# Kernel tuning notes

Hardware: AMD Instinct MI355X
Metric: run time of the kernel (lower is better)

## Reference

```python
import jax, jax.numpy as jnp
import numpy as np

C_SKIP = 64       # channels of a and of b (concat -> 128)
C_OUT = 64
N = 131072        # coarse nodes
E = 1048576       # directed edges (avg degree 8)
N_FINE = 4 * N    # fine mesh nodes after unpool
K = 3 * N_FINE    # unpool scatter assignments


def setup_inputs() -> dict:
    key = jax.random.key(0)
    ks = jax.random.split(key, 9)
    return {
        "a": jax.random.normal(ks[0], (C_SKIP, N), dtype=jnp.float32),
        "b": jax.random.normal(ks[1], (C_SKIP, N), dtype=jnp.float32),
        "W_self": jax.random.normal(ks[2], (C_OUT, 2 * C_SKIP), dtype=jnp.float32) * 0.05,
        "W_neigh": jax.random.normal(ks[3], (C_OUT, 2 * C_SKIP), dtype=jnp.float32) * 0.05,
        "bias": jax.random.normal(ks[4], (C_OUT,), dtype=jnp.float32) * 0.05,
        "gather_index": jax.random.randint(ks[5], (E,), 0, N),
        "reduce_index": jax.random.randint(ks[6], (E,), 0, N),
        "unpool_src": jax.random.randint(ks[7], (K,), 0, N),
        "unpool_dst": jax.random.randint(ks[8], (K,), 0, N_FINE),
    }


def reference(a, b, W_self, W_neigh, bias, gather_index, reduce_index, unpool_src, unpool_dst):
    # concat skip connection along channel dim (-2)
    x = jnp.concatenate((a, b), axis=-2)                  # [C_in, N]
    n = x.shape[-1]
    # GraphConv: gather source features along edges, segment-sum into targets
    msgs = x[:, gather_index]                              # [C_in, E]
    agg = jax.ops.segment_sum(msgs.T, reduce_index, num_segments=n).T  # [C_in, N]
    h = W_self @ x + W_neigh @ agg + bias[:, None]         # [C_out, N]
    h = jax.nn.relu(h)
    # GraphUnpool with reduce='amax': scatter-max coarse features to fine mesh
    out = jnp.zeros((h.shape[0], 4 * n), dtype=h.dtype)
    out = out.at[:, unpool_dst].max(h[:, unpool_src])      # [C_out, N_fine]
    return out
```

## Files before the change

### kernel.cpp

```cpp
#include <hip/hip_runtime.h>
#include <stdint.h>

constexpr int NN = 131072;
constexpr int EE = 1048576;
constexpr int NF = 4 * NN;
constexpr int KK = 3 * NF;

constexpr int NBLK = 256;
constexpr int SH_E = 6;
constexpr int SH_K = 7;
constexpr int NB_E = NN >> SH_E;
constexpr int NB_K = NF >> SH_K;
constexpr int EPT_E = EE / NBLK / 256;
constexpr int EPT_K = KK / NBLK / 256;
constexpr int CAP_E = 2048;
constexpr int CAP_K = 1024;
constexpr int KOFF = NB_E * NBLK;
constexpr int NH   = NB_E * NBLK + NB_K * NBLK;
constexpr int NSCB = NH / 2048;

typedef __attribute__((ext_vector_type(8))) short bf16x8;
typedef __attribute__((ext_vector_type(4))) float f32x4;

__device__ inline uint32_t bf16rn(float f) {
    uint32_t u = __float_as_uint(f);
    return (u + 0x7FFFu + ((u >> 16) & 1u)) >> 16;
}
__device__ inline uint32_t pack2(float lo, float hi) {
    return bf16rn(lo) | (bf16rn(hi) << 16);
}
__device__ inline float bf_lo(uint32_t v) { return __uint_as_float(v << 16); }
__device__ inline float bf_hi(uint32_t v) { return __uint_as_float(v & 0xFFFF0000u); }

__global__ __launch_bounds__(256) void k_transpose(
    const float* __restrict__ a, const float* __restrict__ b,
    uint32_t* __restrict__ xTb)
{
    __shared__ float tile[128][33];
    int i0 = blockIdx.x * 32;
    for (int f = threadIdx.x; f < 128 * 32; f += 256) {
        int c = f >> 5, j = f & 31;
        const float* src = (c < 64) ? a : b;
        tile[c][j] = src[(size_t)(c & 63) * NN + i0 + j];
    }
    __syncthreads();
    for (int f = threadIdx.x; f < 64 * 32; f += 256) {
        int p = f & 63, j = f >> 6;
        xTb[(size_t)(i0 + j) * 64 + p] = pack2(tile[2 * p][j], tile[2 * p + 1][j]);
    }
}

template<int NB, int EPT>
__device__ void pass1_body(const int* __restrict__ idx, int shift,
                           int* __restrict__ histG, int blk, int* hist)
{
    for (int f = threadIdx.x; f < NB; f += 256) hist[f] = 0;
    __syncthreads();
    int base = blk * (256 * EPT);
#pragma unroll
    for (int u = 0; u < EPT; ++u) {
        int b = idx[base + u * 256 + threadIdx.x] >> shift;
        atomicAdd(&hist[b], 1);
    }
    __syncthreads();
    for (int f = threadIdx.x; f < NB; f += 256)
        histG[f * NBLK + blk] = hist[f];
}

__global__ __launch_bounds__(256) void k_pass1(
    const int* __restrict__ reduce_i, const int* __restrict__ up_dst,
    int* __restrict__ histG)
{
    __shared__ int hist[NB_K];
    if (blockIdx.x < NBLK)
        pass1_body<NB_E, EPT_E>(reduce_i, SH_E, histG, blockIdx.x, hist);
    else
        pass1_body<NB_K, EPT_K>(up_dst, SH_K, histG + KOFF, blockIdx.x - NBLK, hist);
}

__global__ __launch_bounds__(256) void k_bsum(
    const int* __restrict__ cnt, int* __restrict__ bsum)
{
    __shared__ int s[256];
    int base = blockIdx.x * 2048;
    int sum = 0;
    for (int j = threadIdx.x; j < 2048; j += 256) sum += cnt[base + j];
    s[threadIdx.x] = sum;
    __syncthreads();
    for (int o = 128; o > 0; o >>= 1) {
        if (threadIdx.x < o) s[threadIdx.x] += s[threadIdx.x + o];
        __syncthreads();
    }
    if (threadIdx.x == 0) bsum[blockIdx.x] = s[0];
}

__global__ __launch_bounds__(256) void k_final(
    int* __restrict__ offs, const int* __restrict__ bsum)
{
    __shared__ int ts[256];
    int partial = 0;
    for (int i = threadIdx.x; i < blockIdx.x; i += 256) partial += bsum[i];
    ts[threadIdx.x] = partial;
    __syncthreads();
    for (int o = 128; o > 0; o >>= 1) {
        if (threadIdx.x < o) ts[threadIdx.x] += ts[threadIdx.x + o];
        __syncthreads();
    }
    int bb = ts[0];
    __syncthreads();

    int base = blockIdx.x * 2048 + threadIdx.x * 8;
    int loc[8];
    int sum = 0;
#pragma unroll
    for (int u = 0; u < 8; ++u) {
        int v = offs[base + u];
        loc[u] = sum;
        sum += v;
    }
    ts[threadIdx.x] = sum;
    __syncthreads();
    for (int o = 1; o < 256; o <<= 1) {
        int v = (threadIdx.x >= o) ? ts[threadIdx.x - o] : 0;
        __syncthreads();
        ts[threadIdx.x] += v;
        __syncthreads();
    }
    int texc = (threadIdx.x == 0) ? 0 : ts[threadIdx.x - 1];
#pragma unroll
    for (int u = 0; u < 8; ++u) offs[base + u] = bb + texc + loc[u];
    if (blockIdx.x == gridDim.x - 1 && threadIdx.x == 255) offs[NH] = bb + ts[255];
}

template<int NB, int EPT>
__device__ void pass2_body(const int* __restrict__ idx,
                           const int* __restrict__ payload, int shift,
                           const int* __restrict__ offsG, int sub,
                           uint32_t* __restrict__ pairs, int blk, int* curs)
{
    for (int f = threadIdx.x; f < NB; f += 256)
        curs[f] = offsG[f * NBLK + blk] - sub;
    __syncthreads();
    int lmask = (1 << shift) - 1;
    int base = blk * (256 * EPT);
#pragma unroll
    for (int u = 0; u < EPT; ++u) {
        int e = base + u * 256 + threadIdx.x;
        int bk = idx[e];
        int pos = atomicAdd(&curs[bk >> shift], 1);
        pairs[pos] = (uint32_t)payload[e] | ((uint32_t)(bk & lmask) << 17);
    }
}

__global__ __launch_bounds__(256) void k_pass2(
    const int* __restrict__ reduce_i, const int* __restrict__ gather_i,
    const int* __restrict__ up_dst, const int* __restrict__ up_src,
    const int* __restrict__ offs,
    uint32_t* __restrict__ pairsE, uint32_t* __restrict__ pairsK)
{
    __shared__ int curs[NB_K];
    if (blockIdx.x < NBLK)
        pass2_body<NB_E, EPT_E>(reduce_i, gather_i, SH_E, offs, 0,
                                pairsE, blockIdx.x, curs);
    else
        pass2_body<NB_K, EPT_K>(up_dst, up_src, SH_K, offs + KOFF, EE,
                                pairsK, blockIdx.x - NBLK, curs);
}

__global__ __launch_bounds__(256) void k_aggcsr(
    const uint32_t* __restrict__ xTb, const int* __restrict__ offsE,
    const uint32_t* __restrict__ pairsE, uint32_t* __restrict__ aggB)
{
    __shared__ uint32_t list[CAP_E];
    __shared__ int offs[65];
    __shared__ int curs[64];
    __shared__ int cnt_s;
    int bin = blockIdx.x;
    if (threadIdx.x == 0) {
        int beg = offsE[bin * NBLK];
        cnt_s = min(offsE[(bin + 1) * NBLK] - beg, CAP_E);
    }
    if (threadIdx.x < 64) curs[threadIdx.x] = 0;
    __syncthreads();
    int beg = offsE[bin * NBLK];
    int cnt = cnt_s;
    for (int i = threadIdx.x; i < cnt; i += 256)
        atomicAdd(&curs[(pairsE[beg + i] >> 17) & 63], 1);
    __syncthreads();
    if (threadIdx.x == 0) {
        int run = 0;
        for (int j = 0; j < 64; ++j) {
            offs[j] = run;
            run += curs[j];
            curs[j] = offs[j];
        }
        offs[64] = run;
    }
    __syncthreads();
    for (int i = threadIdx.x; i < cnt; i += 256) {
        uint32_t u = pairsE[beg + i];
        int p = atomicAdd(&curs[(u >> 17) & 63], 1);
        list[p] = u;
    }
    __syncthreads();

    int w = threadIdx.x >> 6, lane = threadIdx.x & 63;
    int n0 = w * 16, n1 = n0 + 16;
    int e0 = offs[n0], e1 = offs[n1];
    size_t rowbase = (size_t)(bin * 64) * 64 + lane;
    float sx = 0.f, sy = 0.f;
    int cur = n0;
    for (int e = e0; e < e1; e += 16) {
        int nb = e1 - e;
        uint32_t pr[16], v[16];
#pragma unroll
        for (int j = 0; j < 16; ++j)
            pr[j] = list[e + ((j < nb) ? j : (nb - 1))];
#pragma unroll
        for (int j = 0; j < 16; ++j)
            v[j] = xTb[(size_t)(pr[j] & 0x1FFFF) * 64 + lane];
#pragma unroll
        for (int j = 0; j < 16; ++j) {
            if (j < nb) {
                int d = (pr[j] >> 17) & 63;
                if (d != cur) {
                    aggB[rowbase + (size_t)cur * 64] = pack2(sx, sy);
                    for (int z = cur + 1; z < d; ++z)
                        aggB[rowbase + (size_t)z * 64] = 0u;
                    cur = d;
                    sx = 0.f; sy = 0.f;
                }
                sx += bf_lo(v[j]);
                sy += bf_hi(v[j]);
            }
        }
    }
    aggB[rowbase + (size_t)cur * 64] = pack2(sx, sy);
    for (int z = cur + 1; z < n1; ++z)
        aggB[rowbase + (size_t)z * 64] = 0u;
}

__global__ __launch_bounds__(256) void k_gemm(
    const uint32_t* __restrict__ xTb, const uint32_t* __restrict__ aggB,
    const float* __restrict__ Wself, const float* __restrict__ Wneigh,
    const float* __restrict__ bias, uint32_t* __restrict__ hT)
{
    int lane = threadIdx.x & 63;
    int wid = blockIdx.x * 4 + (threadIdx.x >> 6);
    int lr = lane & 15, lq = lane >> 4;

    bf16x8 wf[4][8];
#pragma unroll
    for (int mt = 0; mt < 4; ++mt) {
#pragma unroll
        for (int kt = 0; kt < 8; ++kt) {
            const float* W = (kt < 4) ? Wself : Wneigh;
            const float* p = W + (size_t)(mt * 16 + lr) * 128 + (kt & 3) * 32 + lq * 8;
            bf16x8 v;
#pragma unroll
            for (int j = 0; j < 8; ++j) v[j] = (short)bf16rn(p[j]);
            wf[mt][kt] = v;
        }
    }
    float bv[4][4];
#pragma unroll
    for (int mt = 0; mt < 4; ++mt)
#pragma unroll
        for (int r = 0; r < 4; ++r)
            bv[mt][r] = bias[mt * 16 + lq * 4 + r];

    const int NG = NN / 16;
    int stride = gridDim.x * 4;
    for (int g = wid; g < NG; g += stride) {
        int n = g * 16 + lr;
        const uint32_t* xr = xTb + (size_t)n * 64 + lq * 4;
        const uint32_t* ar = aggB + (size_t)n * 64 + lq * 4;
        bf16x8 bq[8];
#pragma unroll
        for (int kt = 0; kt < 4; ++kt)
            bq[kt] = *reinterpret_cast<const bf16x8*>(xr + kt * 16);
#pragma unroll
        for (int kt = 0; kt < 4; ++kt)
            bq[4 + kt] = *reinterpret_cast<const bf16x8*>(ar + kt * 16);
#pragma unroll
        for (int mt = 0; mt < 4; ++mt) {
            f32x4 acc = {0.f, 0.f, 0.f, 0.f};
#pragma unroll
            for (int kt = 0; kt < 8; ++kt)
                acc = __builtin_amdgcn_mfma_f32_16x16x32_bf16(wf[mt][kt], bq[kt], acc, 0, 0, 0);
            uint32_t u0 = pack2(fmaxf(acc[0] + bv[mt][0], 0.f), fmaxf(acc[1] + bv[mt][1], 0.f));
            uint32_t u1 = pack2(fmaxf(acc[2] + bv[mt][2], 0.f), fmaxf(acc[3] + bv[mt][3], 0.f));
            *reinterpret_cast<uint2*>(hT + (size_t)n * 32 + mt * 8 + lq * 2) = make_uint2(u0, u1);
        }
    }
}

__global__ __launch_bounds__(256) void k_unpoolcsr(
    const uint16_t* __restrict__ hT16, const int* __restrict__ offsK,
    const uint32_t* __restrict__ pairsK, float* __restrict__ out)
{
    __shared__ uint32_t list[CAP_K];
    __shared__ int offs[129];
    __shared__ int curs[128];
    __shared__ uint16_t buf[128][65];
    __shared__ int cnt_s;
    int bin = blockIdx.x;
    if (threadIdx.x == 0) {
        int beg = offsK[bin * NBLK] - EE;
        cnt_s = min(offsK[(bin + 1) * NBLK] - EE - beg, CAP_K);
    }
    if (threadIdx.x < 128) curs[threadIdx.x] = 0;
    for (int f = threadIdx.x; f < 128 * 65; f += 256) ((uint16_t*)buf)[f] = 0;
    __syncthreads();
    int beg = offsK[bin * NBLK] - EE;
    int cnt = cnt_s;
    for (int i = threadIdx.x; i < cnt; i += 256)
        atomicAdd(&curs[(pairsK[beg + i] >> 17) & 127], 1);
    __syncthreads();
    if (threadIdx.x == 0) {
        int run = 0;
        for (int j = 0; j < 128; ++j) {
            offs[j] = run;
            run += curs[j];
            curs[j] = offs[j];
        }
        offs[128] = run;
    }
    __syncthreads();
    for (int i = threadIdx.x; i < cnt; i += 256) {
        uint32_t u = pairsK[beg + i];
        int p = atomicAdd(&curs[(u >> 17) & 127], 1);
        list[p] = u;
    }
    __syncthreads();

    int w = threadIdx.x >> 6, lane = threadIdx.x & 63;
    int n0 = w * 32, n1 = n0 + 32;
    int e0 = offs[n0], e1 = offs[n1];
    uint32_t m = 0;
    int cur = n0;
    for (int e = e0; e < e1; e += 16) {
        int nb = e1 - e;
        uint32_t pr[16], v[16];
#pragma unroll
        for (int j = 0; j < 16; ++j)
            pr[j] = list[e + ((j < nb) ? j : (nb - 1))];
#pragma unroll
        for (int j = 0; j < 16; ++j)
            v[j] = hT16[(size_t)(pr[j] & 0x1FFFF) * 64 + lane];
#pragma unroll
        for (int j = 0; j < 16; ++j) {
            if (j < nb) {
                int d = (pr[j] >> 17) & 127;
                if (d != cur) {
                    buf[cur][lane] = (uint16_t)m;
                    cur = d;
                    m = 0;
                }
                m = max(m, v[j]);
            }
        }
    }
    buf[cur][lane] = (uint16_t)m;
    __syncthreads();
    int j0 = bin << 7;
    for (int f = threadIdx.x; f < 64 * 128; f += 256) {
        int c = f >> 7, j = f & 127;
        out[(size_t)c * NF + j0 + j] = __uint_as_float(((uint32_t)buf[j][c]) << 16);
    }
}

extern "C" void kernel_launch(void* const* d_in, const int* in_sizes, int n_in,
                              void* d_out, int out_size, void* d_ws, size_t ws_size,
                              hipStream_t stream)
{
    const float* a      = (const float*)d_in[0];
    const float* b      = (const float*)d_in[1];
    const float* Wself  = (const float*)d_in[2];
    const float* Wneigh = (const float*)d_in[3];
    const float* bias   = (const float*)d_in[4];
    const int* gather_i = (const int*)d_in[5];
    const int* reduce_i = (const int*)d_in[6];
    const int* up_src   = (const int*)d_in[7];
    const int* up_dst   = (const int*)d_in[8];
    float* out = (float*)d_out;

    uint32_t* xTb   = (uint32_t*)d_ws;
    uint32_t* aggB  = xTb + (size_t)NN * 64;
    uint32_t* hT    = aggB + (size_t)NN * 64;
    uint32_t* pairsK= hT + (size_t)NN * 32;
    int* offs       = (int*)(pairsK + KK);
    int* bsum       = offs + (size_t)NH + 1;
    uint32_t* pairsE= hT;

    size_t need = ((size_t)NN * 160 + KK + (size_t)NH + 1 + NSCB) * 4;
    if (ws_size < need) return;

    k_transpose<<<NN / 32, 256, 0, stream>>>(a, b, xTb);

    k_pass1<<<2 * NBLK, 256, 0, stream>>>(reduce_i, up_dst, offs);
    k_bsum<<<NSCB, 256, 0, stream>>>(offs, bsum);
    k_final<<<NSCB, 256, 0, stream>>>(offs, bsum);
    k_pass2<<<2 * NBLK, 256, 0, stream>>>(reduce_i, gather_i, up_dst, up_src,
                                          offs, pairsE, pairsK);

    k_aggcsr<<<NB_E, 256, 0, stream>>>(xTb, offs, pairsE, aggB);

    k_gemm<<<512, 256, 0, stream>>>(xTb, aggB, Wself, Wneigh, bias, hT);

    k_unpoolcsr<<<NB_K, 256, 0, stream>>>((const uint16_t*)hT, offs + KOFF,
                                          pairsK, out);
}
```

Measured before the change: 264.3 us.

## Fuse transpose with histogram pass and use 1024-thread blocks for binning

Merges the input transpose kernel and the histogram pass into one launch, with block ranges dispatched by blockIdx, and cuts the binning partitions from 256 to 64 blocks of 1024 threads. This saves one kernel launch, lets the independent transpose and counting work overlap, and shrinks the per-block offset table that the scan kernels process by four times. In exchange, the sort passes run on only 128 blocks, which may underfill the GPU, and the large blocks limit occupancy.

```diff
diff --git a/kernel.cpp b/kernel.cpp
--- a/kernel.cpp
+++ b/kernel.cpp
@@ -6,18 +6,20 @@
 constexpr int NF = 4 * NN;
 constexpr int KK = 3 * NF;
 
-constexpr int NBLK = 256;
+constexpr int NBLK = 64;
+constexpr int TPS  = 1024;
 constexpr int SH_E = 6;
 constexpr int SH_K = 7;
 constexpr int NB_E = NN >> SH_E;
 constexpr int NB_K = NF >> SH_K;
-constexpr int EPT_E = EE / NBLK / 256;
-constexpr int EPT_K = KK / NBLK / 256;
+constexpr int EPT_E = EE / NBLK / TPS;
+constexpr int EPT_K = KK / NBLK / TPS;
 constexpr int CAP_E = 2048;
 constexpr int CAP_K = 1024;
 constexpr int KOFF = NB_E * NBLK;
 constexpr int NH   = NB_E * NBLK + NB_K * NBLK;
 constexpr int NSCB = NH / 2048;
+constexpr int NTRB = NN / 32 / 4;
 
 typedef __attribute__((ext_vector_type(8))) short bf16x8;
 typedef __attribute__((ext_vector_type(4))) float f32x4;
@@ -32,50 +34,53 @@
 __device__ inline float bf_lo(uint32_t v) { return __uint_as_float(v << 16); }
 __device__ inline float bf_hi(uint32_t v) { return __uint_as_float(v & 0xFFFF0000u); }
 
-__global__ __launch_bounds__(256) void k_transpose(
-    const float* __restrict__ a, const float* __restrict__ b,
-    uint32_t* __restrict__ xTb)
-{
-    __shared__ float tile[128][33];
-    int i0 = blockIdx.x * 32;
-    for (int f = threadIdx.x; f < 128 * 32; f += 256) {
-        int c = f >> 5, j = f & 31;
-        const float* src = (c < 64) ? a : b;
-        tile[c][j] = src[(size_t)(c & 63) * NN + i0 + j];
-    }
-    __syncthreads();
-    for (int f = threadIdx.x; f < 64 * 32; f += 256) {
-        int p = f & 63, j = f >> 6;
-        xTb[(size_t)(i0 + j) * 64 + p] = pack2(tile[2 * p][j], tile[2 * p + 1][j]);
-    }
-}
-
 template<int NB, int EPT>
 __device__ void pass1_body(const int* __restrict__ idx, int shift,
                            int* __restrict__ histG, int blk, int* hist)
 {
-    for (int f = threadIdx.x; f < NB; f += 256) hist[f] = 0;
-    __syncthreads();
-    int base = blk * (256 * EPT);
+    for (int f = threadIdx.x; f < NB; f += TPS) hist[f] = 0;
+    __syncthreads();
+    int base = blk * (TPS * EPT);
 #pragma unroll
     for (int u = 0; u < EPT; ++u) {
-        int b = idx[base + u * 256 + threadIdx.x] >> shift;
+        int b = idx[base + u * TPS + threadIdx.x] >> shift;
         atomicAdd(&hist[b], 1);
     }
     __syncthreads();
-    for (int f = threadIdx.x; f < NB; f += 256)
+    for (int f = threadIdx.x; f < NB; f += TPS)
         histG[f * NBLK + blk] = hist[f];
 }
 
-__global__ __launch_bounds__(256) void k_pass1(
+__global__ __launch_bounds__(1024) void k_fused1(
+    const float* __restrict__ a, const float* __restrict__ b,
+    uint32_t* __restrict__ xTb,
     const int* __restrict__ reduce_i, const int* __restrict__ up_dst,
     int* __restrict__ histG)
 {
-    __shared__ int hist[NB_K];
-    if (blockIdx.x < NBLK)
-        pass1_body<NB_E, EPT_E>(reduce_i, SH_E, histG, blockIdx.x, hist);
-    else
-        pass1_body<NB_K, EPT_K>(up_dst, SH_K, histG + KOFF, blockIdx.x - NBLK, hist);
+    __shared__ int smem[128 * 33];
+    if (blockIdx.x < NTRB) {
+        float (*tile)[33] = (float (*)[33])smem;
+        for (int t = 0; t < 4; ++t) {
+            int i0 = (blockIdx.x * 4 + t) * 32;
+            for (int f = threadIdx.x; f < 128 * 32; f += TPS) {
+                int c = f >> 5, j = f & 31;
+                const float* src = (c < 64) ? a : b;
+                tile[c][j] = src[(size_t)(c & 63) * NN + i0 + j];
+            }
+            __syncthreads();
+            for (int f = threadIdx.x; f < 64 * 32; f += TPS) {
+                int p = f & 63, j = f >> 6;
+                xTb[(size_t)(i0 + j) * 64 + p] =
+                    pack2(tile[2 * p][j], tile[2 * p + 1][j]);
+            }
+            __syncthreads();
+        }
+    } else if (blockIdx.x < NTRB + NBLK) {
+        pass1_body<NB_E, EPT_E>(reduce_i, SH_E, histG, blockIdx.x - NTRB, smem);
+    } else {
+        pass1_body<NB_K, EPT_K>(up_dst, SH_K, histG + KOFF,
+                                blockIdx.x - NTRB - NBLK, smem);
+    }
 }
 
 __global__ __launch_bounds__(256) void k_bsum(
@@ -138,21 +143,21 @@
                            const int* __restrict__ offsG, int sub,
                            uint32_t* __restrict__ pairs, int blk, int* curs)
 {
-    for (int f = threadIdx.x; f < NB; f += 256)
+    for (int f = threadIdx.x; f < NB; f += TPS)
         curs[f] = offsG[f * NBLK + blk] - sub;
     __syncthreads();
     int lmask = (1 << shift) - 1;
-    int base = blk * (256 * EPT);
+    int base = blk * (TPS * EPT);
 #pragma unroll
     for (int u = 0; u < EPT; ++u) {
-        int e = base + u * 256 + threadIdx.x;
+        int e = base + u * TPS + threadIdx.x;
         int bk = idx[e];
         int pos = atomicAdd(&curs[bk >> shift], 1);
         pairs[pos] = (uint32_t)payload[e] | ((uint32_t)(bk & lmask) << 17);
     }
 }
 
-__global__ __launch_bounds__(256) void k_pass2(
+__global__ __launch_bounds__(1024) void k_pass2(
     const int* __restrict__ reduce_i, const int* __restrict__ gather_i,
     const int* __restrict__ up_dst, const int* __restrict__ up_src,
     const int* __restrict__ offs,
@@ -396,12 +401,12 @@
     size_t need = ((size_t)NN * 160 + KK + (size_t)NH + 1 + NSCB) * 4;
     if (ws_size < need) return;
 
-    k_transpose<<<NN / 32, 256, 0, stream>>>(a, b, xTb);
-
-    k_pass1<<<2 * NBLK, 256, 0, stream>>>(reduce_i, up_dst, offs);
+    k_fused1<<<NTRB + 2 * NBLK, TPS, 0, stream>>>(a, b, xTb, reduce_i, up_dst, offs);
+
     k_bsum<<<NSCB, 256, 0, stream>>>(offs, bsum);
     k_final<<<NSCB, 256, 0, stream>>>(offs, bsum);
-    k_pass2<<<2 * NBLK, 256, 0, stream>>>(reduce_i, gather_i, up_dst, up_src,
+
+    k_pass2<<<2 * NBLK, TPS, 0, stream>>>(reduce_i, gather_i, up_dst, up_src,
                                           offs, pairsE, pairsK);
 
     k_aggcsr<<<NB_E, 256, 0, stream>>>(xTb, offs, pairsE, aggB);
```

After: 272.2 us. 1.03x slower.
